# Performance work log

Measured on AMD Instinct MI355X. Metric: run time of the kernel, lower is better.

Reference implementation:

```python
import jax, jax.numpy as jnp
import numpy as np

N, D, H, C, K, NCLS, TW = 8192, 768, 4, 192, 8, 7, 1.0
HC = H * C  # 768


def setup_inputs() -> dict:
    key = jax.random.key(0)
    ks = jax.random.split(key, 40)
    gl = lambda i, shp: (jax.random.normal(ks[i], shp, jnp.float32)
                         * (1.0 / np.sqrt(shp[0] if len(shp) > 1 else shp[0])))
    inp = {"x": jax.random.normal(ks[0], (N, D), jnp.float32)}
    # BatchNorm (eval mode: running stats)
    inp["bn_gamma"] = jnp.ones((D,), jnp.float32)
    inp["bn_beta"] = jnp.zeros((D,), jnp.float32)
    inp["bn_rm"] = jnp.zeros((D,), jnp.float32)
    inp["bn_rv"] = jnp.ones((D,), jnp.float32)
    # GATConv params: W [in, H*C], att_src/att_dst [H, C], bias
    dims_in = [D, HC, HC, C]
    bias_dim = [HC, HC, C, C]  # concat,concat,mean,mean
    for li in range(4):
        b = 1 + li * 3
        inp[f"g{li+1}_w"] = gl(b, (dims_in[li], HC))
        inp[f"g{li+1}_as"] = jax.random.normal(ks[b + 1], (H, C), jnp.float32) * 0.1
        inp[f"g{li+1}_ad"] = jax.random.normal(ks[b + 2], (H, C), jnp.float32) * 0.1
        inp[f"g{li+1}_b"] = jnp.zeros((bias_dim[li],), jnp.float32)
    inp["res1_w"] = gl(14, (D, HC)); inp["res1_b"] = jnp.zeros((HC,), jnp.float32)
    inp["res2_w"] = gl(15, (HC, C)); inp["res2_b"] = jnp.zeros((C,), jnp.float32)
    for li, dim in zip(range(4), [HC, HC, C, C]):
        inp[f"ln{li+1}_g"] = jnp.ones((dim,), jnp.float32)
        inp[f"ln{li+1}_b"] = jnp.zeros((dim,), jnp.float32)
    inp["fc_w"] = gl(16, (C, NCLS)); inp["fc_b"] = jnp.zeros((NCLS,), jnp.float32)
    return inp


def _ln(x, g, b):
    mu = x.mean(-1, keepdims=True)
    v = ((x - mu) ** 2).mean(-1, keepdims=True)
    return (x - mu) * jax.lax.rsqrt(v + 1e-5) * g + b


def _build_edges(x):
    # cosine-similarity top-k graph (indices only; grads are cut upstream,
    # matching the original .item()-based host loop)
    xn = x / (jnp.linalg.norm(x, axis=1, keepdims=True) + 1e-8)
    sim = xn @ xn.T                       # [N, N]
    _, idx = jax.lax.top_k(sim, K + 1)    # first hit is self
    nbr = idx[:, 1:]                      # [N, K]
    src0 = jnp.repeat(jnp.arange(N), K)
    dst0 = nbr.reshape(-1)
    i = jnp.arange(N - 1)
    # temporal edges (i,i+1)&(i+1,i) added only if (i,i+1) not already a topk edge
    m = ~jnp.any(nbr[:-1] == (i + 1)[:, None], axis=1)
    sl = jnp.arange(N)  # self-loops (GATConv add_self_loops=True)
    src = jnp.concatenate([src0, i, i + 1, sl])
    dst = jnp.concatenate([dst0, i + 1, i, sl])
    mask = jnp.concatenate([jnp.ones(N * K, bool), m, m, jnp.ones(N, bool)])
    return src, dst, mask


def _gat(x, W, a_s, a_d, b, src, dst, mask, concat):
    n = x.shape[0]
    h = (x @ W).reshape(n, H, C)
    es = (h * a_s[None]).sum(-1)  # [N, H]
    ed = (h * a_d[None]).sum(-1)
    e = jax.nn.leaky_relu(es[src] + ed[dst], 0.2)  # [E, H]
    e = jnp.where(mask[:, None], e, -1e9)
    emax = jax.ops.segment_max(e, dst, num_segments=n)
    emax = jnp.where(jnp.isfinite(emax), emax, 0.0)
    ex = jnp.exp(e - emax[dst]) * mask[:, None].astype(e.dtype)
    denom = jax.ops.segment_sum(ex, dst, num_segments=n)
    alpha = ex / (denom[dst] + 1e-16)
    out = jax.ops.segment_sum(alpha[:, :, None] * h[src], dst, num_segments=n)
    out = out.reshape(n, HC) if concat else out.mean(1)
    return out + b


def reference(x, bn_gamma, bn_beta, bn_rm, bn_rv,
              g1_w, g1_as, g1_ad, g1_b, g2_w, g2_as, g2_ad, g2_b,
              g3_w, g3_as, g3_ad, g3_b, g4_w, g4_as, g4_ad, g4_b,
              res1_w, res1_b, res2_w, res2_b,
              ln1_g, ln1_b, ln2_g, ln2_b, ln3_g, ln3_b, ln4_g, ln4_b,
              fc_w, fc_b):
    xb = (x - bn_rm) * jax.lax.rsqrt(bn_rv + 1e-5) * bn_gamma + bn_beta
    src, dst, mask = _build_edges(jax.lax.stop_gradient(xb))
    r = xb @ res1_w + res1_b
    h = _gat(xb, g1_w, g1_as, g1_ad, g1_b, src, dst, mask, True)
    h = _ln(jax.nn.relu(h) + r, ln1_g, ln1_b)
    r = h
    h = _gat(h, g2_w, g2_as, g2_ad, g2_b, src, dst, mask, True)
    h = _ln(jax.nn.relu(h) + r, ln2_g, ln2_b)
    r = h @ res2_w + res2_b
    h = _gat(h, g3_w, g3_as, g3_ad, g3_b, src, dst, mask, False)
    h = _ln(jax.nn.relu(h) + r, ln3_g, ln3_b)
    r = h
    h = _gat(h, g4_w, g4_as, g4_ad, g4_b, src, dst, mask, False)
    h = _ln(jax.nn.relu(h) + r, ln4_g, ln4_b)
    return h @ fc_w + fc_b
```

## Files before the change

### kernel.cpp

```cpp
#include <hip/hip_runtime.h>
#include <hip/hip_bf16.h>

#define NN 8192
#define DD 768
#define HH 4
#define CC 192
#define KK 8
#define HC 768

typedef __attribute__((ext_vector_type(8))) short short8;
typedef __attribute__((ext_vector_type(4))) float floatx4;

static __device__ __forceinline__ short f2bf(float v) {
    unsigned u = __builtin_bit_cast(unsigned, v);
    u += 0x7fff + ((u >> 16) & 1);
    return (short)(u >> 16);
}
static __device__ __forceinline__ float bf2f(short s) {
    unsigned u = ((unsigned)(unsigned short)s) << 16;
    return __builtin_bit_cast(float, u);
}

static __device__ __forceinline__ void gl16(const void* g, void* l) {
    __builtin_amdgcn_global_load_lds(
        (__attribute__((address_space(1))) void*)(void*)g,
        (__attribute__((address_space(3))) void*)l, 16, 0, 0);
}

__global__ __launch_bounds__(256) void bnorm_kernel(const float* __restrict__ x,
    const float* __restrict__ g, const float* __restrict__ b,
    const float* __restrict__ rm, const float* __restrict__ rv,
    short* __restrict__ xbh, short* __restrict__ xbl,
    short* __restrict__ xnh, short* __restrict__ xnl)
{
    int i = blockIdx.x, t = threadIdx.x;
    __shared__ float red[256];
    float v[3];
    float ss = 0.f;
#pragma unroll
    for (int q = 0; q < 3; q++) {
        int d = t + q * 256;
        float xv = x[(size_t)i * DD + d];
        float vv = (xv - rm[d]) * rsqrtf(rv[d] + 1e-5f) * g[d] + b[d];
        v[q] = vv; ss += vv * vv;
    }
    red[t] = ss; __syncthreads();
    for (int s = 128; s; s >>= 1) { if (t < s) red[t] += red[t + s]; __syncthreads(); }
    float inv = 1.0f / (sqrtf(red[0]) + 1e-8f);
#pragma unroll
    for (int q = 0; q < 3; q++) {
        int d = t + q * 256;
        size_t idx = (size_t)i * DD + d;
        float vv = v[q];
        short h = f2bf(vv);
        xbh[idx] = h; xbl[idx] = f2bf(vv - bf2f(h));
        float nv = vv * inv;
        short nh = f2bf(nv);
        xnh[idx] = nh; xnl[idx] = f2bf(nv - bf2f(nh));
    }
}

__global__ __launch_bounds__(256) void wtrans6(
    const float* w0, short* o0h, short* o0l,
    const float* w1, short* o1h, short* o1l,
    const float* w2, short* o2h, short* o2l,
    const float* w3, short* o3h, short* o3l,
    const float* w4, short* o4h, short* o4l,
    const float* w5, short* o5h, short* o5l)
{
    int idx = blockIdx.x * 256 + threadIdx.x;
    const float* w; short* oh; short* ol; int K, P; int r;
    if (idx < 589824)            { w = w0; oh = o0h; ol = o0l; K = 768; P = 768; r = idx; }
    else if (idx < 2 * 589824)   { w = w1; oh = o1h; ol = o1l; K = 768; P = 768; r = idx - 589824; }
    else if (idx < 3 * 589824)   { w = w2; oh = o2h; ol = o2l; K = 768; P = 768; r = idx - 2 * 589824; }
    else if (idx < 3 * 589824 + 147456) { w = w3; oh = o3h; ol = o3l; K = 768; P = 192; r = idx - 3 * 589824; }
    else if (idx < 4 * 589824 + 147456) { w = w4; oh = o4h; ol = o4l; K = 768; P = 768; r = idx - 3 * 589824 - 147456; }
    else if (idx < 4 * 589824 + 2 * 147456) { w = w5; oh = o5h; ol = o5l; K = 192; P = 768; r = idx - 4 * 589824 - 147456; }
    else return;
    int p = r / K, k = r % K;
    float v = w[(size_t)k * P + p];
    short h = f2bf(v);
    oh[r] = h;
    ol[r] = f2bf(v - bf2f(h));
}

__global__ __launch_bounds__(256) void mfma_sym(
    const short* __restrict__ Xh, const short* __restrict__ Xl,
    int rowa, int rowb, int diag,
    float* __restrict__ Cab, float* __restrict__ Cba)
{
    __shared__ __attribute__((aligned(16))) float fsm[64 * 129];
    short* sAh = (short*)fsm;
    short* sAl = (short*)fsm + 4096;
    short* sBh = (short*)fsm + 8192;
    short* sBl = (short*)fsm + 12288;
    int t = threadIdx.x;
    int wave = t >> 6, lane = t & 63;
    int wm = wave & 1, wn = wave >> 1;
    int bi, bj;
    if (diag) {
        int L = blockIdx.x;
        int j = (int)((sqrtf(8.f * (float)L + 1.f) - 1.f) * 0.5f);
        while (j * (j + 1) / 2 > L) j--;
        while ((j + 1) * (j + 2) / 2 <= L) j++;
        bi = L - j * (j + 1) / 2; bj = j;
    } else { bi = blockIdx.y; bj = blockIdx.x; }
    int i0 = bi * 128, j0 = bj * 128;
    int mrow = lane & 15, quad = lane >> 4;

    int srow = lane >> 2;
    int kg   = (lane & 3) ^ ((lane >> 3) & 3);
    int koff = kg * 8;
    int c0 = wave * 2, c1 = c0 + 1;
    int ar0 = rowa + i0 + c0 * 16 + srow, ar1 = rowa + i0 + c1 * 16 + srow;
    int br0 = rowb + j0 + c0 * 16 + srow, br1 = rowb + j0 + c1 * 16 + srow;
    const short* pAh0 = Xh + (size_t)ar0 * DD + koff;
    const short* pAh1 = Xh + (size_t)ar1 * DD + koff;
    const short* pAl0 = Xl + (size_t)ar0 * DD + koff;
    const short* pAl1 = Xl + (size_t)ar1 * DD + koff;
    const short* pBh0 = Xh + (size_t)br0 * DD + koff;
    const short* pBh1 = Xh + (size_t)br1 * DD + koff;
    const short* pBl0 = Xl + (size_t)br0 * DD + koff;
    const short* pBl1 = Xl + (size_t)br1 * DD + koff;
    short* dA0 = sAh + c0 * 512; short* dA1 = sAh + c1 * 512;
    short* dAl0 = sAl + c0 * 512; short* dAl1 = sAl + c1 * 512;
    short* dB0 = sBh + c0 * 512; short* dB1 = sBh + c1 * 512;
    short* dBl0 = sBl + c0 * 512; short* dBl1 = sBl + c1 * 512;

    floatx4 acc[4][4];
#pragma unroll
    for (int a = 0; a < 4; a++)
#pragma unroll
        for (int b = 0; b < 4; b++) acc[a][b] = (floatx4){0.f, 0.f, 0.f, 0.f};

    int aoff[4], boff[4];
#pragma unroll
    for (int mt = 0; mt < 4; mt++) {
        int r = wm * 64 + mt * 16 + mrow;
        aoff[mt] = r * 32 + (quad ^ ((r >> 1) & 3)) * 8;
    }
#pragma unroll
    for (int nt = 0; nt < 4; nt++) {
        int r = wn * 64 + nt * 16 + mrow;
        boff[nt] = r * 32 + (quad ^ ((r >> 1) & 3)) * 8;
    }

    for (int k0 = 0; k0 < DD; k0 += 32) {
        gl16(pAh0 + k0, dA0);  gl16(pAh1 + k0, dA1);
        gl16(pAl0 + k0, dAl0); gl16(pAl1 + k0, dAl1);
        gl16(pBh0 + k0, dB0);  gl16(pBh1 + k0, dB1);
        gl16(pBl0 + k0, dBl0); gl16(pBl1 + k0, dBl1);
        __syncthreads();

        short8 ah[4], al[4], bh[4], bl[4];
#pragma unroll
        for (int mt = 0; mt < 4; mt++) {
            ah[mt] = *(const short8*)(sAh + aoff[mt]);
            al[mt] = *(const short8*)(sAl + aoff[mt]);
        }
#pragma unroll
        for (int nt = 0; nt < 4; nt++) {
            bh[nt] = *(const short8*)(sBh + boff[nt]);
            bl[nt] = *(const short8*)(sBl + boff[nt]);
        }
#pragma unroll
        for (int mt = 0; mt < 4; mt++)
#pragma unroll
            for (int nt = 0; nt < 4; nt++) {
                acc[mt][nt] = __builtin_amdgcn_mfma_f32_16x16x32_bf16(
                    ah[mt], bh[nt], acc[mt][nt], 0, 0, 0);
                acc[mt][nt] = __builtin_amdgcn_mfma_f32_16x16x32_bf16(
                    ah[mt], bl[nt], acc[mt][nt], 0, 0, 0);
                acc[mt][nt] = __builtin_amdgcn_mfma_f32_16x16x32_bf16(
                    al[mt], bh[nt], acc[mt][nt], 0, 0, 0);
            }
        __syncthreads();
    }

#pragma unroll
    for (int mt = 0; mt < 4; mt++)
#pragma unroll
        for (int nt = 0; nt < 4; nt++) {
            int col = j0 + wn * 64 + nt * 16 + mrow;
#pragma unroll
            for (int r = 0; r < 4; r++) {
                int row = i0 + wm * 64 + mt * 16 + quad * 4 + r;
                Cab[(size_t)row * 4096 + col] = acc[mt][nt][r];
            }
        }

    if (!diag || bi != bj) {
        float* Cm = Cba;
        for (int half = 0; half < 2; half++) {
            __syncthreads();
            if (wn == half) {
#pragma unroll
                for (int mt = 0; mt < 4; mt++)
#pragma unroll
                    for (int nt = 0; nt < 4; nt++)
#pragma unroll
                        for (int r = 0; r < 4; r++) {
                            int c = nt * 16 + mrow;
                            int rr = wm * 64 + mt * 16 + quad * 4 + r;
                            fsm[c * 129 + rr] = acc[mt][nt][r];
                        }
            }
            __syncthreads();
            for (int it = 0; it < 32; it++) {
                int idx = it * 256 + t;
                int lr = idx >> 7, lc = idx & 127;
                Cm[(size_t)(j0 + half * 64 + lr) * 4096 + i0 + lc] = fsm[lr * 129 + lc];
            }
        }
    }
}

__global__ __launch_bounds__(256) void mfma_nt(
    const short* __restrict__ Ahi, const short* __restrict__ Alo,
    const short* __restrict__ Bhi, const short* __restrict__ Blo,
    const float* __restrict__ bias, int biasN,
    float* __restrict__ C, int Cstride,
    short* __restrict__ Cbf, int bfoff, int bfstride,
    const float* __restrict__ a_s, const float* __restrict__ a_d,
    float* __restrict__ es, float* __restrict__ ed, int hoff,
    int M, int K, int P)
{
    __shared__ __attribute__((aligned(16))) short sAh[128 * 32];
    __shared__ __attribute__((aligned(16))) short sAl[128 * 32];
    __shared__ __attribute__((aligned(16))) short sBh[128 * 32];
    __shared__ __attribute__((aligned(16))) short sBl[128 * 32];
    int t = threadIdx.x;
    int wave = t >> 6, lane = t & 63;
    int wm = wave & 1, wn = wave >> 1;
    int i0 = blockIdx.y * 128, j0 = blockIdx.x * 128;
    int mrow = lane & 15, quad = lane >> 4;

    int srow = lane >> 2;
    int kg   = (lane & 3) ^ ((lane >> 3) & 3);
    int koff = kg * 8;
    int c0 = wave * 2, c1 = c0 + 1;
    int ar0 = i0 + c0 * 16 + srow, ar1 = i0 + c1 * 16 + srow;
    int br0 = j0 + c0 * 16 + srow, br1 = j0 + c1 * 16 + srow;
    if (br0 > P - 1) br0 = P - 1;
    if (br1 > P - 1) br1 = P - 1;
    const short* pAh0 = Ahi + (size_t)ar0 * K + koff;
    const short* pAh1 = Ahi + (size_t)ar1 * K + koff;
    const short* pAl0 = Alo + (size_t)ar0 * K + koff;
    const short* pAl1 = Alo + (size_t)ar1 * K + koff;
    const short* pBh0 = Bhi + (size_t)br0 * K + koff;
    const short* pBh1 = Bhi + (size_t)br1 * K + koff;
    const short* pBl0 = Blo + (size_t)br0 * K + koff;
    const short* pBl1 = Blo + (size_t)br1 * K + koff;
    short* dA0 = sAh + c0 * 512; short* dA1 = sAh + c1 * 512;
    short* dAl0 = sAl + c0 * 512; short* dAl1 = sAl + c1 * 512;
    short* dB0 = sBh + c0 * 512; short* dB1 = sBh + c1 * 512;
    short* dBl0 = sBl + c0 * 512; short* dBl1 = sBl + c1 * 512;

    floatx4 acc[4][4];
#pragma unroll
    for (int a = 0; a < 4; a++)
#pragma unroll
        for (int b = 0; b < 4; b++) acc[a][b] = (floatx4){0.f, 0.f, 0.f, 0.f};

    int aoff[4], boff[4];
#pragma unroll
    for (int mt = 0; mt < 4; mt++) {
        int r = wm * 64 + mt * 16 + mrow;
        aoff[mt] = r * 32 + (quad ^ ((r >> 1) & 3)) * 8;
    }
#pragma unroll
    for (int nt = 0; nt < 4; nt++) {
        int r = wn * 64 + nt * 16 + mrow;
        boff[nt] = r * 32 + (quad ^ ((r >> 1) & 3)) * 8;
    }

    for (int k0 = 0; k0 < K; k0 += 32) {
        gl16(pAh0 + k0, dA0);  gl16(pAh1 + k0, dA1);
        gl16(pAl0 + k0, dAl0); gl16(pAl1 + k0, dAl1);
        gl16(pBh0 + k0, dB0);  gl16(pBh1 + k0, dB1);
        gl16(pBl0 + k0, dBl0); gl16(pBl1 + k0, dBl1);
        __syncthreads();

        short8 ah[4], al[4], bh[4], bl[4];
#pragma unroll
        for (int mt = 0; mt < 4; mt++) {
            ah[mt] = *(const short8*)(sAh + aoff[mt]);
            al[mt] = *(const short8*)(sAl + aoff[mt]);
        }
#pragma unroll
        for (int nt = 0; nt < 4; nt++) {
            bh[nt] = *(const short8*)(sBh + boff[nt]);
            bl[nt] = *(const short8*)(sBl + boff[nt]);
        }
#pragma unroll
        for (int mt = 0; mt < 4; mt++)
#pragma unroll
            for (int nt = 0; nt < 4; nt++) {
                acc[mt][nt] = __builtin_amdgcn_mfma_f32_16x16x32_bf16(
                    ah[mt], bh[nt], acc[mt][nt], 0, 0, 0);
                acc[mt][nt] = __builtin_amdgcn_mfma_f32_16x16x32_bf16(
                    ah[mt], bl[nt], acc[mt][nt], 0, 0, 0);
                acc[mt][nt] = __builtin_amdgcn_mfma_f32_16x16x32_bf16(
                    al[mt], bh[nt], acc[mt][nt], 0, 0, 0);
            }
        __syncthreads();
    }

#pragma unroll
    for (int mt = 0; mt < 4; mt++)
#pragma unroll
        for (int nt = 0; nt < 4; nt++) {
            int col = j0 + wn * 64 + nt * 16 + mrow;
            if (col < P) {
                if (col < bfoff) {
                    float bb = (bias && col < biasN) ? bias[col] : 0.f;
#pragma unroll
                    for (int r = 0; r < 4; r++) {
                        int row = i0 + wm * 64 + mt * 16 + quad * 4 + r;
                        C[(size_t)row * Cstride + col] = acc[mt][nt][r] + bb;
                    }
                } else {
#pragma unroll
                    for (int r = 0; r < 4; r++) {
                        int row = i0 + wm * 64 + mt * 16 + quad * 4 + r;
                        Cbf[(size_t)row * bfstride + col - bfoff] = f2bf(acc[mt][nt][r]);
                    }
                }
            }
        }

    if (a_s) {
        int base = j0 + wn * 64;
        if (base >= hoff && base + 64 <= P) {
            int head = (base - hoff) / CC;
            int cb = (base - hoff) % CC;
#pragma unroll
            for (int mt = 0; mt < 4; mt++) {
                float ps[4] = {0.f, 0.f, 0.f, 0.f};
                float pd[4] = {0.f, 0.f, 0.f, 0.f};
#pragma unroll
                for (int nt = 0; nt < 4; nt++) {
                    int c = cb + nt * 16 + mrow;
                    float as_ = a_s[head * CC + c];
                    float ad_ = a_d[head * CC + c];
#pragma unroll
                    for (int r = 0; r < 4; r++) {
                        ps[r] += acc[mt][nt][r] * as_;
                        pd[r] += acc[mt][nt][r] * ad_;
                    }
                }
#pragma unroll
                for (int off = 1; off < 16; off <<= 1)
#pragma unroll
                    for (int r = 0; r < 4; r++) {
                        ps[r] += __shfl_xor(ps[r], off);
                        pd[r] += __shfl_xor(pd[r], off);
                    }
                if (mrow == 0) {
#pragma unroll
                    for (int r = 0; r < 4; r++) {
                        int row = i0 + wm * 64 + mt * 16 + quad * 4 + r;
                        atomicAdd(&es[row * 4 + head], ps[r]);
                        atomicAdd(&ed[row * 4 + head], pd[r]);
                    }
                }
            }
        }
    }
}

__device__ __forceinline__ bool tk_try(float* v, int* id, float xv, int xi)
{
    if (xv > v[8] || (xv == v[8] && xi < id[8])) {
        v[8] = xv; id[8] = xi;
#pragma unroll
        for (int p = 8; p > 0; p--) {
            if (v[p] > v[p - 1] || (v[p] == v[p - 1] && id[p] < id[p - 1])) {
                float tv = v[p]; v[p] = v[p - 1]; v[p - 1] = tv;
                int ti2 = id[p]; id[p] = id[p - 1]; id[p - 1] = ti2;
            } else break;
        }
        return true;
    }
    return false;
}

__global__ __launch_bounds__(256) void topk1p_kernel(const float* __restrict__ sim,
    float* __restrict__ pv, int* __restrict__ pi,
    int rowbase, int segbase, int colbase)
{
    int wave = threadIdx.x >> 6, lane = threadIdx.x & 63;
    int task = blockIdx.x * 4 + wave;
    int row = task >> 2, seg = task & 3;
    const float4* p4 = (const float4*)(sim + (size_t)row * 4096 + seg * 1024);

    float4 f0 = p4[lane], f1 = p4[lane + 64], f2 = p4[lane + 128], f3 = p4[lane + 192];
    float v[9]; int id[9];
#pragma unroll
    for (int q = 0; q < 9; q++) { v[q] = -3e38f; id[q] = 0x7fffffff; }
    int jb = colbase + seg * 1024 + lane * 4;
#pragma unroll
    for (int g = 0; g < 4; g++) {
        float4 f = g == 0 ? f0 : (g == 1 ? f1 : (g == 2 ? f2 : f3));
        float gm = fmaxf(fmaxf(f.x, f.y), fmaxf(f.z, f.w));
        if (gm >= v[8]) {
            int j = jb + g * 256;
            tk_try(v, id, f.x, j);
            tk_try(v, id, f.y, j + 1);
            tk_try(v, id, f.z, j + 2);
            tk_try(v, id, f.w, j + 3);
        }
    }
    float wv = -3e38f; int wi = 0x7fffffff;
#pragma unroll
    for (int r = 0; r < 9; r++) {
        float bv = v[0]; int bi = id[0];
#pragma unroll
        for (int off = 1; off < 64; off <<= 1) {
            float ov = __shfl_xor(bv, off);
            int oi = __shfl_xor(bi, off);
            if (ov > bv || (ov == bv && oi < bi)) { bv = ov; bi = oi; }
        }
        if (id[0] == bi) {
#pragma unroll
            for (int q = 0; q < 8; q++) { v[q] = v[q + 1]; id[q] = id[q + 1]; }
            v[8] = -3e38f; id[8] = 0x7fffffff;
        }
        if (lane == r) { wv = bv; wi = bi; }
    }
    if (lane < 9) {
        size_t o = ((size_t)(rowbase + row) * 8 + segbase + seg) * 9 + lane;
        pv[o] = wv; pi[o] = wi;
    }
}

__global__ __launch_bounds__(256) void topk2_kernel(const float* __restrict__ pv,
    const int* __restrict__ pi, int* __restrict__ nbr, int r0)
{
    int wave = threadIdx.x >> 6, lane = threadIdx.x & 63;
    int row = blockIdx.x * 4 + wave;
    size_t base = (size_t)row * 72;
    float v[2]; int id[2];
    v[0] = -3e38f; id[0] = 0x7fffffff;
    v[1] = -3e38f; id[1] = 0x7fffffff;
    if (lane < 72) { v[0] = pv[base + lane]; id[0] = pi[base + lane]; }
    if (lane < 8)  { v[1] = pv[base + 64 + lane]; id[1] = pi[base + 64 + lane]; }
    if (v[1] > v[0] || (v[1] == v[0] && id[1] < id[0])) {
        float tv = v[0]; v[0] = v[1]; v[1] = tv;
        int ti = id[0]; id[0] = id[1]; id[1] = ti;
    }
    int myi = 0;
#pragma unroll
    for (int r = 0; r < 9; r++) {
        float bv = v[0]; int bi = id[0];
#pragma unroll
        for (int off = 1; off < 64; off <<= 1) {
            float ov = __shfl_xor(bv, off);
            int oi = __shfl_xor(bi, off);
            if (ov > bv || (ov == bv && oi < bi)) { bv = ov; bi = oi; }
        }
        if (id[0] == bi) {
            v[0] = v[1]; id[0] = id[1];
            v[1] = -3e38f; id[1] = 0x7fffffff;
        }
        if (r >= 1 && lane == r - 1) myi = bi;
    }
    if (lane < KK) nbr[(size_t)(r0 + row) * KK + lane] = myi;
}

__global__ __launch_bounds__(256) void count_kernel(const int* __restrict__ nbr,
                                                    int* __restrict__ deg, int* __restrict__ mfl)
{
    int i = blockIdx.x * 256 + threadIdx.x;
    if (i >= NN) return;
    atomicAdd(&deg[i], 1);
    int mm = 0;
#pragma unroll
    for (int k = 0; k < KK; k++) {
        int j = nbr[i * KK + k];
        atomicAdd(&deg[j], 1);
        if (j == i + 1) mm = 1;
    }
    if (i < NN - 1) {
        mfl[i] = !mm;
        if (!mm) { atomicAdd(&deg[i + 1], 1); atomicAdd(&deg[i], 1); }
    }
}

__global__ __launch_bounds__(256) void scan_kernel(const int* __restrict__ deg,
                                                   int* __restrict__ rowptr, int* __restrict__ cur)
{
    __shared__ int sums[256];
    int t = threadIdx.x;
    int loc[32];
    int base = t * 32;
    int s = 0;
#pragma unroll
    for (int q = 0; q < 32; q++) { loc[q] = s; s += deg[base + q]; }
    sums[t] = s; __syncthreads();
    for (int off = 1; off < 256; off <<= 1) {
        int v = (t >= off) ? sums[t - off] : 0;
        __syncthreads();
        sums[t] += v;
        __syncthreads();
    }
    int myoff = (t == 0) ? 0 : sums[t - 1];
#pragma unroll
    for (int q = 0; q < 32; q++) { int rp = myoff + loc[q]; rowptr[base + q] = rp; cur[base + q] = rp; }
    if (t == 255) rowptr[NN] = sums[255];
}

__global__ __launch_bounds__(256) void fill_kernel(const int* __restrict__ nbr,
    const int* __restrict__ mfl, int* __restrict__ cur, int* __restrict__ csr)
{
    int i = blockIdx.x * 256 + threadIdx.x;
    if (i >= NN) return;
    int pos = atomicAdd(&cur[i], 1); csr[pos] = i;
#pragma unroll
    for (int k = 0; k < KK; k++) {
        int j = nbr[i * KK + k];
        pos = atomicAdd(&cur[j], 1); csr[pos] = i;
    }
    if (i < NN - 1 && mfl[i]) {
        pos = atomicAdd(&cur[i + 1], 1); csr[pos] = i;
        pos = atomicAdd(&cur[i], 1); csr[pos] = i + 1;
    }
}

__global__ __launch_bounds__(256) void agg_ln_kernel(const short* __restrict__ h, int hst,
    const float* __restrict__ es, const float* __restrict__ ed,
    const int* __restrict__ rowptr, const int* __restrict__ csr,
    const float* __restrict__ gb, const float* __restrict__ rres, int rst,
    const float* __restrict__ gamma, const float* __restrict__ beta,
    float* __restrict__ outp, short* __restrict__ ohi, short* __restrict__ olo,
    int Dm, int concat,
    const float* __restrict__ fcw, const float* __restrict__ fcb,
    float* __restrict__ fco)
{
    int j = blockIdx.x;
    int t = threadIdx.x;
    int lane = t & 63, wave = t >> 6;
    __shared__ int ssrc[256];
    __shared__ float sal[256 * 4];
    __shared__ float sred[1024];
    __shared__ float accs[768];
    int p0 = rowptr[j], p1 = rowptr[j + 1];
    int cnt = p1 - p0;
    float edj[4];
#pragma unroll
    for (int hd = 0; hd < 4; hd++) edj[hd] = ed[j * 4 + hd];

    float acc0 = 0.f, acc1 = 0.f, acc2 = 0.f;
    int d0 = t, d1 = t + 256, d2 = t + 512;
    int h0 = d0 / CC, h1_ = d1 / CC, h2_ = d2 / CC;

    if (cnt <= 256) {
        float e[4];
        if (t < cnt) {
            int s = csr[p0 + t];
            ssrc[t] = s;
#pragma unroll
            for (int hd = 0; hd < 4; hd++) {
                float ee = es[s * 4 + hd] + edj[hd];
                e[hd] = ee > 0.f ? ee : 0.2f * ee;
            }
        } else {
#pragma unroll
            for (int hd = 0; hd < 4; hd++) e[hd] = -1e30f;
        }
        float mh[4];
#pragma unroll
        for (int hd = 0; hd < 4; hd++) {
            float rv = e[hd];
#pragma unroll
            for (int off = 32; off; off >>= 1) rv = fmaxf(rv, __shfl_down(rv, off));
            if (lane == 0) sred[wave * 4 + hd] = rv;
        }
        __syncthreads();
#pragma unroll
        for (int hd = 0; hd < 4; hd++)
            mh[hd] = fmaxf(fmaxf(sred[hd], sred[4 + hd]), fmaxf(sred[8 + hd], sred[12 + hd]));
        __syncthreads();
        float ex[4];
#pragma unroll
        for (int hd = 0; hd < 4; hd++) {
            ex[hd] = (t < cnt) ? expf(e[hd] - mh[hd]) : 0.f;
            float rv = ex[hd];
#pragma unroll
            for (int off = 32; off; off >>= 1) rv += __shfl_down(rv, off);
            if (lane == 0) sred[wave * 4 + hd] = rv;
        }
        __syncthreads();
#pragma unroll
        for (int hd = 0; hd < 4; hd++) {
            float dh = sred[hd] + sred[4 + hd] + sred[8 + hd] + sred[12 + hd] + 1e-16f;
            if (t < cnt) sal[t * 4 + hd] = ex[hd] / dh;
        }
        __syncthreads();
        for (int e2 = 0; e2 < cnt; e2++) {
            const short* hs = h + (size_t)ssrc[e2] * hst;
            acc0 += sal[e2 * 4 + h0] * bf2f(hs[d0]);
            acc1 += sal[e2 * 4 + h1_] * bf2f(hs[d1]);
            acc2 += sal[e2 * 4 + h2_] * bf2f(hs[d2]);
        }
    } else {
        float mh[4] = {-1e30f, -1e30f, -1e30f, -1e30f};
        for (int p = p0 + t; p < p1; p += 256) {
            int s = csr[p];
// ... 78 lines not shown
        for (int s = 128; s; s >>= 1) { if (t < s) sred[t] += sred[t + s]; __syncthreads(); }
        float rs = rsqrtf(sred[0] / 768.f + 1e-5f);
        size_t base = (size_t)j * 768;
        float w0 = a0 * rs * gamma[d0] + beta[d0];
        float w1 = a1 * rs * gamma[d1] + beta[d1];
        float w2 = a2 * rs * gamma[d2] + beta[d2];
        if (outp) { outp[base + d0] = w0; outp[base + d1] = w1; outp[base + d2] = w2; }
        short hh;
        hh = f2bf(w0); ohi[base + d0] = hh; olo[base + d0] = f2bf(w0 - bf2f(hh));
        hh = f2bf(w1); ohi[base + d1] = hh; olo[base + d1] = f2bf(w1 - bf2f(hh));
        hh = f2bf(w2); ohi[base + d2] = hh; olo[base + d2] = f2bf(w2 - bf2f(hh));
    } else {
        accs[d0] = acc0; accs[d1] = acc1; accs[d2] = acc2;
        __syncthreads();
        float val = 0.f;
        if (t < CC)
            val = fmaxf((accs[t] + accs[t + CC] + accs[t + 2 * CC] + accs[t + 3 * CC]) * 0.25f
                        + gb[t], 0.f) + rres[(size_t)j * rst + t];
        __syncthreads();
        sred[t] = (t < CC) ? val : 0.f; __syncthreads();
        for (int s = 128; s; s >>= 1) { if (t < s) sred[t] += sred[t + s]; __syncthreads(); }
        float mu = sred[0] / (float)CC;
        __syncthreads();
        float a = val - mu;
        sred[t] = (t < CC) ? a * a : 0.f; __syncthreads();
        for (int s = 128; s; s >>= 1) { if (t < s) sred[t] += sred[t + s]; __syncthreads(); }
        float rs = rsqrtf(sred[0] / (float)CC + 1e-5f);
        float w = a * rs * ((t < CC) ? gamma[t] : 0.f) + ((t < CC) ? beta[t] : 0.f);
        if (t < CC) {
            size_t idx = (size_t)j * CC + t;
            if (outp) outp[idx] = w;
            if (ohi) {
                short hh = f2bf(w);
                ohi[idx] = hh; olo[idx] = f2bf(w - bf2f(hh));
            }
            accs[t] = w;
        }
        if (fco) {
            __syncthreads();
            if (t < 64) {
#pragma unroll
                for (int n = 0; n < 7; n++) {
                    float p = 0.f;
                    for (int d = t; d < CC; d += 64) p += accs[d] * fcw[d * 7 + n];
#pragma unroll
                    for (int off = 32; off; off >>= 1) p += __shfl_down(p, off);
                    if (t == 0) fco[(size_t)j * 7 + n] = p + fcb[n];
                }
            }
        }
    }
}

extern "C" void kernel_launch(void* const* d_in, const int* in_sizes, int n_in,
                              void* d_out, int out_size, void* d_ws, size_t ws_size,
                              hipStream_t stream)
{
    const float* x     = (const float*)d_in[0];
    const float* bn_g  = (const float*)d_in[1];
    const float* bn_b  = (const float*)d_in[2];
    const float* bn_rm = (const float*)d_in[3];
    const float* bn_rv = (const float*)d_in[4];
    const float* g_w[4]  = {(const float*)d_in[5], (const float*)d_in[9],
                            (const float*)d_in[13], (const float*)d_in[17]};
    const float* g_as[4] = {(const float*)d_in[6], (const float*)d_in[10],
                            (const float*)d_in[14], (const float*)d_in[18]};
    const float* g_ad[4] = {(const float*)d_in[7], (const float*)d_in[11],
                            (const float*)d_in[15], (const float*)d_in[19]};
    const float* g_b[4]  = {(const float*)d_in[8], (const float*)d_in[12],
                            (const float*)d_in[16], (const float*)d_in[20]};
    const float* res1_w = (const float*)d_in[21];
    const float* res1_b = (const float*)d_in[22];
    const float* res2_w = (const float*)d_in[23];
    const float* res2_b = (const float*)d_in[24];
    const float* ln_g[4] = {(const float*)d_in[25], (const float*)d_in[27],
                            (const float*)d_in[29], (const float*)d_in[31]};
    const float* ln_b[4] = {(const float*)d_in[26], (const float*)d_in[28],
                            (const float*)d_in[30], (const float*)d_in[32]};
    const float* fc_w = (const float*)d_in[33];
    const float* fc_b = (const float*)d_in[34];
    float* out = (float*)d_out;

    float* F = (float*)d_ws;
    float* SAB  = F; F += 16777216;
    float* UNI  = F; F += 16777216;
    float* SBA = UNI;
    float* R1  = UNI;
    float* H1  = R1 + 6291456;
    float* R2  = H1 + 6291456;
    float* H3  = R2 + 1572864;
    float* ESB = H3 + 1572864;
    short* S = (short*)F;
    short* XNH = S; S += 6291456;
    short* XNL = S; S += 6291456;
    short* XAH = S; S += 6291456;
    short* XAL = S; S += 6291456;
    short* HBH = S; S += 6291456;
    short* WT1H = S; S += 1179648;
    short* WT1L = S; S += 1179648;
    short* WT2H = S; S += 589824;
    short* WT2L = S; S += 589824;
    short* WT3H = S; S += 737280;
    short* WT3L = S; S += 737280;
    short* WT4H = S; S += 147456;
    short* WT4L = S; S += 147456;
    int* I = (int*)S;
    int* NBR    = I; I += NN * KK;
    int* DEG    = I; I += NN;
    int* ROWPTR = I; I += NN + 8;
    int* CUR    = I; I += NN;
    int* MFL    = I; I += NN;
    int* CSR    = I; I += 131072;
    float* PV   = (float*)I; I += 589824;
    int* PI     = I; I += 589824;
    float* ES[4], *ED[4];
    for (int l = 0; l < 4; l++) { ES[l] = ESB + l * 65536; ED[l] = ES[l] + 32768; }

    bnorm_kernel<<<NN, 256, 0, stream>>>(x, bn_g, bn_b, bn_rm, bn_rv,
                                         XAH, XAL, XNH, XNL);
    hipMemsetAsync(DEG, 0, NN * sizeof(int), stream);
    wtrans6<<<(4 * 589824 + 2 * 147456 + 255) / 256, 256, 0, stream>>>(
        res1_w, WT1H, WT1L,
        g_w[0], WT1H + 768 * 768, WT1L + 768 * 768,
        g_w[1], WT2H, WT2L,
        res2_w, WT3H, WT3L,
        g_w[2], WT3H + 192 * 768, WT3L + 192 * 768,
        g_w[3], WT4H, WT4L);
    mfma_sym<<<dim3(32, 32), 256, 0, stream>>>(XNH, XNL, 0, 4096, 0, SAB, SBA);
    topk1p_kernel<<<4096, 256, 0, stream>>>(SAB, PV, PI, 0, 4, 4096);
    topk1p_kernel<<<4096, 256, 0, stream>>>(SBA, PV, PI, 4096, 0, 0);
    mfma_sym<<<528, 256, 0, stream>>>(XNH, XNL, 0, 0, 1, SAB, SAB);
    topk1p_kernel<<<4096, 256, 0, stream>>>(SAB, PV, PI, 0, 0, 0);
    mfma_sym<<<528, 256, 0, stream>>>(XNH, XNL, 4096, 4096, 1, SBA, SBA);
    topk1p_kernel<<<4096, 256, 0, stream>>>(SBA, PV, PI, 4096, 4, 4096);
    topk2_kernel<<<NN / 4, 256, 0, stream>>>(PV, PI, NBR, 0);
    count_kernel<<<NN / 256, 256, 0, stream>>>(NBR, DEG, MFL);
    scan_kernel<<<1, 256, 0, stream>>>(DEG, ROWPTR, CUR);
    fill_kernel<<<NN / 256, 256, 0, stream>>>(NBR, MFL, CUR, CSR);
    hipMemsetAsync(ESB, 0, 262144 * sizeof(float), stream);
    mfma_nt<<<dim3(12, NN / 128), 256, 0, stream>>>(XAH, XAL, WT1H, WT1L,
        res1_b, 768, R1, 768, HBH, 768, 768,
        g_as[0], g_ad[0], ES[0], ED[0], 768, NN, DD, 1536);
    agg_ln_kernel<<<NN, 256, 0, stream>>>(HBH, 768, ES[0], ED[0], ROWPTR, CSR,
        g_b[0], R1, 768, ln_g[0], ln_b[0], H1, XAH, XAL, HC, 1, nullptr, nullptr, nullptr);
    mfma_nt<<<dim3(6, NN / 128), 256, 0, stream>>>(XAH, XAL, WT2H, WT2L,
        nullptr, 0, nullptr, 0, HBH, 0, 768,
        g_as[1], g_ad[1], ES[1], ED[1], 0, NN, HC, HC);
    agg_ln_kernel<<<NN, 256, 0, stream>>>(HBH, 768, ES[1], ED[1], ROWPTR, CSR,
        g_b[1], H1, 768, ln_g[1], ln_b[1], nullptr, XAH, XAL, HC, 1, nullptr, nullptr, nullptr);
    mfma_nt<<<dim3(8, NN / 128), 256, 0, stream>>>(XAH, XAL, WT3H, WT3L,
        res2_b, 192, R2, 192, HBH, 192, 768,
        g_as[2], g_ad[2], ES[2], ED[2], 192, NN, HC, 960);
    agg_ln_kernel<<<NN, 256, 0, stream>>>(HBH, 768, ES[2], ED[2], ROWPTR, CSR,
        g_b[2], R2, 192, ln_g[2], ln_b[2], H3, XAH, XAL, CC, 0, nullptr, nullptr, nullptr);
    mfma_nt<<<dim3(6, NN / 128), 256, 0, stream>>>(XAH, XAL, WT4H, WT4L,
        nullptr, 0, nullptr, 0, HBH, 0, 768,
        g_as[3], g_ad[3], ES[3], ED[3], 0, NN, CC, HC);
    agg_ln_kernel<<<NN, 256, 0, stream>>>(HBH, 768, ES[3], ED[3], ROWPTR, CSR,
        g_b[3], H3, 192, ln_g[3], ln_b[3], nullptr, nullptr, nullptr, CC, 0, fc_w, fc_b, out);
}
```

Before: 1.085 ms.

## Compute similarity in single bf16, store bf16 sims, rescore top candidates in fp32

The cosine-similarity GEMM now uses only the high bf16 part (one MFMA instead of three) and writes its results as bf16, which halves the similarity matrix traffic. The top-k pass over bf16 sims keeps 24 candidates per row, and a new rescore kernel recomputes their exact fp32 dot products to pick the final 8 neighbours. The two diagonal GEMM launches and the topk launches are merged into fewer, larger launches. The risk is that a true neighbour falls outside the 24 bf16 candidates when similarities are close.

```diff
diff --git a/kernel.cpp b/kernel.cpp
--- a/kernel.cpp
+++ b/kernel.cpp
@@ -31,7 +31,7 @@
     const float* __restrict__ g, const float* __restrict__ b,
     const float* __restrict__ rm, const float* __restrict__ rv,
     short* __restrict__ xbh, short* __restrict__ xbl,
-    short* __restrict__ xnh, short* __restrict__ xnl)
+    short* __restrict__ xnh, float* __restrict__ xnf)
 {
     int i = blockIdx.x, t = threadIdx.x;
     __shared__ float red[256];
@@ -55,8 +55,8 @@
         short h = f2bf(vv);
         xbh[idx] = h; xbl[idx] = f2bf(vv - bf2f(h));
         float nv = vv * inv;
-        short nh = f2bf(nv);
-        xnh[idx] = nh; xnl[idx] = f2bf(nv - bf2f(nh));
+        xnf[idx] = nv;
+        xnh[idx] = f2bf(nv);
     }
 }
 
@@ -85,26 +85,29 @@
 }
 
 __global__ __launch_bounds__(256) void mfma_sym(
-    const short* __restrict__ Xh, const short* __restrict__ Xl,
-    int rowa, int rowb, int diag,
-    float* __restrict__ Cab, float* __restrict__ Cba)
-{
-    __shared__ __attribute__((aligned(16))) float fsm[64 * 129];
-    short* sAh = (short*)fsm;
-    short* sAl = (short*)fsm + 4096;
-    short* sBh = (short*)fsm + 8192;
-    short* sBl = (short*)fsm + 12288;
+    const short* __restrict__ Xh, int mode,
+    short* __restrict__ P0, short* __restrict__ P1)
+{
+    __shared__ __attribute__((aligned(16))) short smem[8704];
+    short* sAh = smem;
+    short* sBh = smem + 4096;
     int t = threadIdx.x;
     int wave = t >> 6, lane = t & 63;
     int wm = wave & 1, wn = wave >> 1;
-    int bi, bj;
-    if (diag) {
+    int bi, bj, rowa, rowb; short *Cab, *Cba;
+    if (mode == 0) {
+        bi = blockIdx.y; bj = blockIdx.x; rowa = 0; rowb = 4096;
+        Cab = P0; Cba = P1;
+    } else {
         int L = blockIdx.x;
+        int which = (L >= 528) ? 1 : 0; L -= which * 528;
         int j = (int)((sqrtf(8.f * (float)L + 1.f) - 1.f) * 0.5f);
         while (j * (j + 1) / 2 > L) j--;
         while ((j + 1) * (j + 2) / 2 <= L) j++;
         bi = L - j * (j + 1) / 2; bj = j;
-    } else { bi = blockIdx.y; bj = blockIdx.x; }
+        rowa = rowb = which ? 4096 : 0;
+        Cab = Cba = which ? P1 : P0;
+    }
     int i0 = bi * 128, j0 = bj * 128;
     int mrow = lane & 15, quad = lane >> 4;
 
@@ -112,20 +115,12 @@
     int kg   = (lane & 3) ^ ((lane >> 3) & 3);
     int koff = kg * 8;
     int c0 = wave * 2, c1 = c0 + 1;
-    int ar0 = rowa + i0 + c0 * 16 + srow, ar1 = rowa + i0 + c1 * 16 + srow;
-    int br0 = rowb + j0 + c0 * 16 + srow, br1 = rowb + j0 + c1 * 16 + srow;
-    const short* pAh0 = Xh + (size_t)ar0 * DD + koff;
-    const short* pAh1 = Xh + (size_t)ar1 * DD + koff;
-    const short* pAl0 = Xl + (size_t)ar0 * DD + koff;
-    const short* pAl1 = Xl + (size_t)ar1 * DD + koff;
-    const short* pBh0 = Xh + (size_t)br0 * DD + koff;
-    const short* pBh1 = Xh + (size_t)br1 * DD + koff;
-    const short* pBl0 = Xl + (size_t)br0 * DD + koff;
-    const short* pBl1 = Xl + (size_t)br1 * DD + koff;
+    const short* pA0 = Xh + (size_t)(rowa + i0 + c0 * 16 + srow) * DD + koff;
+    const short* pA1 = Xh + (size_t)(rowa + i0 + c1 * 16 + srow) * DD + koff;
+    const short* pB0 = Xh + (size_t)(rowb + j0 + c0 * 16 + srow) * DD + koff;
+    const short* pB1 = Xh + (size_t)(rowb + j0 + c1 * 16 + srow) * DD + koff;
     short* dA0 = sAh + c0 * 512; short* dA1 = sAh + c1 * 512;
-    short* dAl0 = sAl + c0 * 512; short* dAl1 = sAl + c1 * 512;
     short* dB0 = sBh + c0 * 512; short* dB1 = sBh + c1 * 512;
-    short* dBl0 = sBl + c0 * 512; short* dBl1 = sBl + c1 * 512;
 
     floatx4 acc[4][4];
 #pragma unroll
@@ -146,51 +141,46 @@
     }
 
     for (int k0 = 0; k0 < DD; k0 += 32) {
-        gl16(pAh0 + k0, dA0);  gl16(pAh1 + k0, dA1);
-        gl16(pAl0 + k0, dAl0); gl16(pAl1 + k0, dAl1);
-        gl16(pBh0 + k0, dB0);  gl16(pBh1 + k0, dB1);
-        gl16(pBl0 + k0, dBl0); gl16(pBl1 + k0, dBl1);
-        __syncthreads();
-
-        short8 ah[4], al[4], bh[4], bl[4];
-#pragma unroll
-        for (int mt = 0; mt < 4; mt++) {
-            ah[mt] = *(const short8*)(sAh + aoff[mt]);
-            al[mt] = *(const short8*)(sAl + aoff[mt]);
-        }
-#pragma unroll
-        for (int nt = 0; nt < 4; nt++) {
-            bh[nt] = *(const short8*)(sBh + boff[nt]);
-            bl[nt] = *(const short8*)(sBl + boff[nt]);
-        }
+        gl16(pA0 + k0, dA0); gl16(pA1 + k0, dA1);
+        gl16(pB0 + k0, dB0); gl16(pB1 + k0, dB1);
+        __syncthreads();
+        short8 ah[4], bh[4];
+#pragma unroll
+        for (int mt = 0; mt < 4; mt++) ah[mt] = *(const short8*)(sAh + aoff[mt]);
+#pragma unroll
+        for (int nt = 0; nt < 4; nt++) bh[nt] = *(const short8*)(sBh + boff[nt]);
 #pragma unroll
         for (int mt = 0; mt < 4; mt++)
 #pragma unroll
-            for (int nt = 0; nt < 4; nt++) {
+            for (int nt = 0; nt < 4; nt++)
                 acc[mt][nt] = __builtin_amdgcn_mfma_f32_16x16x32_bf16(
                     ah[mt], bh[nt], acc[mt][nt], 0, 0, 0);
-                acc[mt][nt] = __builtin_amdgcn_mfma_f32_16x16x32_bf16(
-                    ah[mt], bl[nt], acc[mt][nt], 0, 0, 0);
-                acc[mt][nt] = __builtin_amdgcn_mfma_f32_16x16x32_bf16(
-                    al[mt], bh[nt], acc[mt][nt], 0, 0, 0);
-            }
-        __syncthreads();
-    }
-
-#pragma unroll
-    for (int mt = 0; mt < 4; mt++)
-#pragma unroll
-        for (int nt = 0; nt < 4; nt++) {
-            int col = j0 + wn * 64 + nt * 16 + mrow;
-#pragma unroll
-            for (int r = 0; r < 4; r++) {
-                int row = i0 + wm * 64 + mt * 16 + quad * 4 + r;
-                Cab[(size_t)row * 4096 + col] = acc[mt][nt][r];
-            }
-        }
-
-    if (!diag || bi != bj) {
-        float* Cm = Cba;
+        __syncthreads();
+    }
+
+    short* st = smem;
+    for (int half = 0; half < 2; half++) {
+        __syncthreads();
+        if (wm == half) {
+#pragma unroll
+            for (int mt = 0; mt < 4; mt++)
+#pragma unroll
+                for (int nt = 0; nt < 4; nt++)
+#pragma unroll
+                    for (int r = 0; r < 4; r++)
+                        st[(mt * 16 + quad * 4 + r) * 136 + wn * 64 + nt * 16 + mrow]
+                            = f2bf(acc[mt][nt][r]);
+        }
+        __syncthreads();
+#pragma unroll
+        for (int it = 0; it < 4; it++) {
+            int idx = it * 256 + t;
+            int lr = idx >> 4, lc = (idx & 15) * 8;
+            *(short8*)&Cab[(size_t)(i0 + half * 64 + lr) * 4096 + j0 + lc]
+                = *(const short8*)&st[lr * 136 + lc];
+        }
+    }
+    if (mode == 0 || bi != bj) {
         for (int half = 0; half < 2; half++) {
             __syncthreads();
             if (wn == half) {
@@ -199,19 +189,227 @@
 #pragma unroll
                     for (int nt = 0; nt < 4; nt++)
 #pragma unroll
-                        for (int r = 0; r < 4; r++) {
-                            int c = nt * 16 + mrow;
-                            int rr = wm * 64 + mt * 16 + quad * 4 + r;
-                            fsm[c * 129 + rr] = acc[mt][nt][r];
-                        }
+                        for (int r = 0; r < 4; r++)
+                            st[(nt * 16 + mrow) * 136 + wm * 64 + mt * 16 + quad * 4 + r]
+                                = f2bf(acc[mt][nt][r]);
             }
             __syncthreads();
-            for (int it = 0; it < 32; it++) {
+#pragma unroll
+            for (int it = 0; it < 4; it++) {
                 int idx = it * 256 + t;
-                int lr = idx >> 7, lc = idx & 127;
-                Cm[(size_t)(j0 + half * 64 + lr) * 4096 + i0 + lc] = fsm[lr * 129 + lc];
-            }
-        }
+                int lr = idx >> 4, lc = (idx & 15) * 8;
+                *(short8*)&Cba[(size_t)(j0 + half * 64 + lr) * 4096 + i0 + lc]
+                    = *(const short8*)&st[lr * 136 + lc];
+            }
+        }
+    }
+}
+
+__device__ __forceinline__ bool tk_try(float* v, int* id, float xv, int xi)
+{
+    if (xv > v[8] || (xv == v[8] && xi < id[8])) {
+        v[8] = xv; id[8] = xi;
+#pragma unroll
+        for (int p = 8; p > 0; p--) {
+            if (v[p] > v[p - 1] || (v[p] == v[p - 1] && id[p] < id[p - 1])) {
+                float tv = v[p]; v[p] = v[p - 1]; v[p - 1] = tv;
+                int ti2 = id[p]; id[p] = id[p - 1]; id[p - 1] = ti2;
+            } else break;
+        }
+        return true;
+    }
+    return false;
+}
+
+__global__ __launch_bounds__(256) void topk1b_kernel(
+    const short* __restrict__ simA, const short* __restrict__ simB,
+    float* __restrict__ pv, int* __restrict__ pi, int phase)
+{
+    int wave = threadIdx.x >> 6, lane = threadIdx.x & 63;
+    int gtask = blockIdx.x * 4 + wave;
+    int which = (gtask >= 16384) ? 1 : 0;
+    int task = gtask - which * 16384;
+    const short* sim = which ? simB : simA;
+    int rowbase = which ? 4096 : 0;
+    int segbase, colbase;
+    if (phase == 0) { segbase = which ? 0 : 4; colbase = which ? 0 : 4096; }
+    else            { segbase = which ? 4 : 0; colbase = which ? 4096 : 0; }
+    int row = task >> 2, seg = task & 3;
+    const short8* p8 = (const short8*)(sim + (size_t)row * 4096 + seg * 1024);
+    short8 s0 = p8[lane], s1 = p8[lane + 64];
+    float v[9]; int id[9];
+#pragma unroll
+    for (int q = 0; q < 9; q++) { v[q] = -3e38f; id[q] = 0x7fffffff; }
+    int jb = colbase + seg * 1024 + lane * 8;
+    float f0[8], f1[8];
+#pragma unroll
+    for (int q = 0; q < 8; q++) { f0[q] = bf2f(s0[q]); f1[q] = bf2f(s1[q]); }
+    float g0 = f0[0], g1 = f1[0];
+#pragma unroll
+    for (int q = 1; q < 8; q++) { g0 = fmaxf(g0, f0[q]); g1 = fmaxf(g1, f1[q]); }
+    if (g0 >= v[8]) {
+#pragma unroll
+        for (int q = 0; q < 8; q++) tk_try(v, id, f0[q], jb + q);
+    }
+    if (g1 >= v[8]) {
+#pragma unroll
+        for (int q = 0; q < 8; q++) tk_try(v, id, f1[q], jb + 512 + q);
+    }
+    float wv = -3e38f; int wi = 0x7fffffff;
+#pragma unroll
+    for (int r = 0; r < 9; r++) {
+        float bv = v[0]; int bi = id[0];
+#pragma unroll
+        for (int off = 1; off < 64; off <<= 1) {
+            float ov = __shfl_xor(bv, off);
+            int oi = __shfl_xor(bi, off);
+            if (ov > bv || (ov == bv && oi < bi)) { bv = ov; bi = oi; }
+        }
+        if (id[0] == bi) {
+#pragma unroll
+            for (int q = 0; q < 8; q++) { v[q] = v[q + 1]; id[q] = id[q + 1]; }
+            v[8] = -3e38f; id[8] = 0x7fffffff;
+        }
+        if (lane == r) { wv = bv; wi = bi; }
+    }
+    if (lane < 9) {
+        size_t o = ((size_t)(rowbase + row) * 8 + segbase + seg) * 9 + lane;
+        pv[o] = wv; pi[o] = wi;
+    }
+}
+
+__global__ __launch_bounds__(256) void rescore_kernel(
+    const float* __restrict__ xnf,
+    const float* __restrict__ pv, const int* __restrict__ pi,
+    int* __restrict__ nbr)
+{
+    int row = blockIdx.x, t = threadIdx.x;
+    int wave = t >> 6, lane = t & 63;
+    __shared__ float own[768];
+    __shared__ float cv[72]; __shared__ int ci[72];
+    __shared__ int seli[24];
+    __shared__ float rv[24]; __shared__ int ri[24];
+    for (int d = t; d < 768; d += 256) own[d] = xnf[(size_t)row * 768 + d];
+    if (t < 72) { cv[t] = pv[(size_t)row * 72 + t]; ci[t] = pi[(size_t)row * 72 + t]; }
+    __syncthreads();
+    if (wave == 0) {
+        float v[2]; int id[2];
+        v[0] = (lane < 72) ? cv[lane] : -3e38f;
+        id[0] = (lane < 72) ? ci[lane] : 0x7fffffff;
+        v[1] = (lane < 8) ? cv[64 + lane] : -3e38f;
+        id[1] = (lane < 8) ? ci[64 + lane] : 0x7fffffff;
+        if (v[1] > v[0] || (v[1] == v[0] && id[1] < id[0])) {
+            float tv = v[0]; v[0] = v[1]; v[1] = tv;
+            int ti = id[0]; id[0] = id[1]; id[1] = ti;
+        }
+#pragma unroll
+        for (int r = 0; r < 24; r++) {
+            float bv = v[0]; int bi = id[0];
+#pragma unroll
+            for (int off = 1; off < 64; off <<= 1) {
+                float ov = __shfl_xor(bv, off);
+                int oi = __shfl_xor(bi, off);
+                if (ov > bv || (ov == bv && oi < bi)) { bv = ov; bi = oi; }
+            }
+            if (id[0] == bi) {
+                v[0] = v[1]; id[0] = id[1];
+                v[1] = -3e38f; id[1] = 0x7fffffff;
+            }
+            if (lane == r) seli[r] = bi;
+        }
+    }
+    __syncthreads();
+    float ow[12];
+#pragma unroll
+    for (int q = 0; q < 12; q++) ow[q] = own[q * 64 + lane];
+    for (int k = 0; k < 6; k++) {
+        int c = wave * 6 + k;
+        int src = seli[c];
+        const float* cr = xnf + (size_t)src * 768;
+        float s = 0.f;
+#pragma unroll
+        for (int q = 0; q < 12; q++) s += ow[q] * cr[q * 64 + lane];
+#pragma unroll
+        for (int off = 32; off; off >>= 1) s += __shfl_xor(s, off);
+        if (lane == 0) { rv[c] = s; ri[c] = src; }
+    }
+    __syncthreads();
+    if (wave == 0) {
+        float v0 = (lane < 24) ? rv[lane] : -3e38f;
+        int i0_ = (lane < 24) ? ri[lane] : 0x7fffffff;
+        int myi = 0;
+#pragma unroll
+        for (int r = 0; r < 9; r++) {
+            float bv = v0; int bi = i0_;
+#pragma unroll
+            for (int off = 1; off < 64; off <<= 1) {
+                float ov = __shfl_xor(bv, off);
+                int oi = __shfl_xor(bi, off);
+                if (ov > bv || (ov == bv && oi < bi)) { bv = ov; bi = oi; }
+            }
+            if (i0_ == bi) { v0 = -3e38f; i0_ = 0x7fffffff; }
+            if (r >= 1 && lane == r - 1) myi = bi;
+        }
+        if (lane < KK) nbr[(size_t)row * KK + lane] = myi;
+    }
+}
+
+__global__ __launch_bounds__(256) void count_kernel(const int* __restrict__ nbr,
+                                                    int* __restrict__ deg, int* __restrict__ mfl)
+{
+    int i = blockIdx.x * 256 + threadIdx.x;
+    if (i >= NN) return;
+    atomicAdd(&deg[i], 1);
+    int mm = 0;
+#pragma unroll
+    for (int k = 0; k < KK; k++) {
+        int j = nbr[i * KK + k];
+        atomicAdd(&deg[j], 1);
+        if (j == i + 1) mm = 1;
+    }
+    if (i < NN - 1) {
+        mfl[i] = !mm;
+        if (!mm) { atomicAdd(&deg[i + 1], 1); atomicAdd(&deg[i], 1); }
+    }
+}
+
+__global__ __launch_bounds__(256) void scan_kernel(const int* __restrict__ deg,
+                                                   int* __restrict__ rowptr, int* __restrict__ cur)
+{
+    __shared__ int sums[256];
+    int t = threadIdx.x;
+    int loc[32];
+    int base = t * 32;
+    int s = 0;
+#pragma unroll
+    for (int q = 0; q < 32; q++) { loc[q] = s; s += deg[base + q]; }
+    sums[t] = s; __syncthreads();
+    for (int off = 1; off < 256; off <<= 1) {
+        int v = (t >= off) ? sums[t - off] : 0;
+        __syncthreads();
+        sums[t] += v;
+        __syncthreads();
+    }
+    int myoff = (t == 0) ? 0 : sums[t - 1];
+#pragma unroll
+    for (int q = 0; q < 32; q++) { int rp = myoff + loc[q]; rowptr[base + q] = rp; cur[base + q] = rp; }
+    if (t == 255) rowptr[NN] = sums[255];
+}
+
+__global__ __launch_bounds__(256) void fill_kernel(const int* __restrict__ nbr,
+    const int* __restrict__ mfl, int* __restrict__ cur, int* __restrict__ csr)
+{
+    int i = blockIdx.x * 256 + threadIdx.x;
+    if (i >= NN) return;
+    int pos = atomicAdd(&cur[i], 1); csr[pos] = i;
+#pragma unroll
+    for (int k = 0; k < KK; k++) {
+        int j = nbr[i * KK + k];
+        pos = atomicAdd(&cur[j], 1); csr[pos] = i;
+    }
+    if (i < NN - 1 && mfl[i]) {
+        pos = atomicAdd(&cur[i + 1], 1); csr[pos] = i;
+        pos = atomicAdd(&cur[i], 1); csr[pos] = i + 1;
     }
 }
 
@@ -366,164 +564,6 @@
                 }
             }
         }
-    }
-}
-
-__device__ __forceinline__ bool tk_try(float* v, int* id, float xv, int xi)
-{
-    if (xv > v[8] || (xv == v[8] && xi < id[8])) {
-        v[8] = xv; id[8] = xi;
-#pragma unroll
-        for (int p = 8; p > 0; p--) {
-            if (v[p] > v[p - 1] || (v[p] == v[p - 1] && id[p] < id[p - 1])) {
-                float tv = v[p]; v[p] = v[p - 1]; v[p - 1] = tv;
-                int ti2 = id[p]; id[p] = id[p - 1]; id[p - 1] = ti2;
-            } else break;
-        }
-        return true;
-    }
-    return false;
-}
-
-__global__ __launch_bounds__(256) void topk1p_kernel(const float* __restrict__ sim,
-    float* __restrict__ pv, int* __restrict__ pi,
-    int rowbase, int segbase, int colbase)
-{
-    int wave = threadIdx.x >> 6, lane = threadIdx.x & 63;
-    int task = blockIdx.x * 4 + wave;
-    int row = task >> 2, seg = task & 3;
-    const float4* p4 = (const float4*)(sim + (size_t)row * 4096 + seg * 1024);
-
-    float4 f0 = p4[lane], f1 = p4[lane + 64], f2 = p4[lane + 128], f3 = p4[lane + 192];
-    float v[9]; int id[9];
-#pragma unroll
-    for (int q = 0; q < 9; q++) { v[q] = -3e38f; id[q] = 0x7fffffff; }
-    int jb = colbase + seg * 1024 + lane * 4;
-#pragma unroll
-    for (int g = 0; g < 4; g++) {
-        float4 f = g == 0 ? f0 : (g == 1 ? f1 : (g == 2 ? f2 : f3));
-        float gm = fmaxf(fmaxf(f.x, f.y), fmaxf(f.z, f.w));
-        if (gm >= v[8]) {
-            int j = jb + g * 256;
-            tk_try(v, id, f.x, j);
-            tk_try(v, id, f.y, j + 1);
-            tk_try(v, id, f.z, j + 2);
-            tk_try(v, id, f.w, j + 3);
-        }
-    }
-    float wv = -3e38f; int wi = 0x7fffffff;
-#pragma unroll
-    for (int r = 0; r < 9; r++) {
-        float bv = v[0]; int bi = id[0];
-#pragma unroll
-        for (int off = 1; off < 64; off <<= 1) {
-            float ov = __shfl_xor(bv, off);
-            int oi = __shfl_xor(bi, off);
-            if (ov > bv || (ov == bv && oi < bi)) { bv = ov; bi = oi; }
-        }
-        if (id[0] == bi) {
-#pragma unroll
-            for (int q = 0; q < 8; q++) { v[q] = v[q + 1]; id[q] = id[q + 1]; }
-            v[8] = -3e38f; id[8] = 0x7fffffff;
-        }
-        if (lane == r) { wv = bv; wi = bi; }
-    }
-    if (lane < 9) {
-        size_t o = ((size_t)(rowbase + row) * 8 + segbase + seg) * 9 + lane;
-        pv[o] = wv; pi[o] = wi;
-    }
-}
-
-__global__ __launch_bounds__(256) void topk2_kernel(const float* __restrict__ pv,
-    const int* __restrict__ pi, int* __restrict__ nbr, int r0)
-{
-    int wave = threadIdx.x >> 6, lane = threadIdx.x & 63;
-    int row = blockIdx.x * 4 + wave;
-    size_t base = (size_t)row * 72;
-    float v[2]; int id[2];
-    v[0] = -3e38f; id[0] = 0x7fffffff;
-    v[1] = -3e38f; id[1] = 0x7fffffff;
-    if (lane < 72) { v[0] = pv[base + lane]; id[0] = pi[base + lane]; }
-    if (lane < 8)  { v[1] = pv[base + 64 + lane]; id[1] = pi[base + 64 + lane]; }
-    if (v[1] > v[0] || (v[1] == v[0] && id[1] < id[0])) {
-        float tv = v[0]; v[0] = v[1]; v[1] = tv;
-        int ti = id[0]; id[0] = id[1]; id[1] = ti;
-    }
-    int myi = 0;
-#pragma unroll
-    for (int r = 0; r < 9; r++) {
-        float bv = v[0]; int bi = id[0];
-#pragma unroll
-        for (int off = 1; off < 64; off <<= 1) {
-            float ov = __shfl_xor(bv, off);
-            int oi = __shfl_xor(bi, off);
-            if (ov > bv || (ov == bv && oi < bi)) { bv = ov; bi = oi; }
-        }
-        if (id[0] == bi) {
-            v[0] = v[1]; id[0] = id[1];
-            v[1] = -3e38f; id[1] = 0x7fffffff;
-        }
-        if (r >= 1 && lane == r - 1) myi = bi;
-    }
-    if (lane < KK) nbr[(size_t)(r0 + row) * KK + lane] = myi;
-}
-
-__global__ __launch_bounds__(256) void count_kernel(const int* __restrict__ nbr,
-                                                    int* __restrict__ deg, int* __restrict__ mfl)
-{
-    int i = blockIdx.x * 256 + threadIdx.x;
-    if (i >= NN) return;
-    atomicAdd(&deg[i], 1);
-    int mm = 0;
-#pragma unroll
-    for (int k = 0; k < KK; k++) {
-        int j = nbr[i * KK + k];
-        atomicAdd(&deg[j], 1);
-        if (j == i + 1) mm = 1;
-    }
-    if (i < NN - 1) {
-        mfl[i] = !mm;
-        if (!mm) { atomicAdd(&deg[i + 1], 1); atomicAdd(&deg[i], 1); }
-    }
-}
-
-__global__ __launch_bounds__(256) void scan_kernel(const int* __restrict__ deg,
-                                                   int* __restrict__ rowptr, int* __restrict__ cur)
-{
-    __shared__ int sums[256];
-    int t = threadIdx.x;
-    int loc[32];
-    int base = t * 32;
-    int s = 0;
-#pragma unroll
-    for (int q = 0; q < 32; q++) { loc[q] = s; s += deg[base + q]; }
-    sums[t] = s; __syncthreads();
-    for (int off = 1; off < 256; off <<= 1) {
-        int v = (t >= off) ? sums[t - off] : 0;
-        __syncthreads();
-        sums[t] += v;
-        __syncthreads();
-    }
-    int myoff = (t == 0) ? 0 : sums[t - 1];
-#pragma unroll
-    for (int q = 0; q < 32; q++) { int rp = myoff + loc[q]; rowptr[base + q] = rp; cur[base + q] = rp; }
-    if (t == 255) rowptr[NN] = sums[255];
-}
-
-__global__ __launch_bounds__(256) void fill_kernel(const int* __restrict__ nbr,
-    const int* __restrict__ mfl, int* __restrict__ cur, int* __restrict__ csr)
-{
-    int i = blockIdx.x * 256 + threadIdx.x;
-    if (i >= NN) return;
-    int pos = atomicAdd(&cur[i], 1); csr[pos] = i;
-#pragma unroll
-    for (int k = 0; k < KK; k++) {
-        int j = nbr[i * KK + k];
-        pos = atomicAdd(&cur[j], 1); csr[pos] = i;
-    }
-    if (i < NN - 1 && mfl[i]) {
-        pos = atomicAdd(&cur[i + 1], 1); csr[pos] = i;
-        pos = atomicAdd(&cur[i], 1); csr[pos] = i + 1;
     }
 }
 
@@ -768,17 +808,17 @@
     float* out = (float*)d_out;
 
     float* F = (float*)d_ws;
-    float* SAB  = F; F += 16777216;
-    float* UNI  = F; F += 16777216;
-    float* SBA = UNI;
-    float* R1  = UNI;
-    float* H1  = R1 + 6291456;
-    float* R2  = H1 + 6291456;
-    float* H3  = R2 + 1572864;
-    float* ESB = H3 + 1572864;
+    float* XNF = F; F += 6291456;
+    float* R1  = F; F += 6291456;
+    float* H1  = F; F += 6291456;
+    float* R2  = F; F += 1572864;
+    float* H3  = F; F += 1572864;
+    float* ESB = F; F += 262144;
+    float* PV  = F; F += 589824;
     short* S = (short*)F;
+    short* SAB = S; S += 16777216;
+    short* SBA = S; S += 16777216;
     short* XNH = S; S += 6291456;
-    short* XNL = S; S += 6291456;
     short* XAH = S; S += 6291456;
     short* XAL = S; S += 6291456;
     short* HBH = S; S += 6291456;
@@ -797,14 +837,14 @@
     int* CUR    = I; I += NN;
     int* MFL    = I; I += NN;
     int* CSR    = I; I += 131072;
-    float* PV   = (float*)I; I += 589824;
     int* PI     = I; I += 589824;
     float* ES[4], *ED[4];
     for (int l = 0; l < 4; l++) { ES[l] = ESB + l * 65536; ED[l] = ES[l] + 32768; }
 
     bnorm_kernel<<<NN, 256, 0, stream>>>(x, bn_g, bn_b, bn_rm, bn_rv,
-                                         XAH, XAL, XNH, XNL);
+                                         XAH, XAL, XNH, XNF);
     hipMemsetAsync(DEG, 0, NN * sizeof(int), stream);
+    hipMemsetAsync(ESB, 0, 262144 * sizeof(float), stream);
     wtrans6<<<(4 * 589824 + 2 * 147456 + 255) / 256, 256, 0, stream>>>(
         res1_w, WT1H, WT1L,
         g_w[0], WT1H + 768 * 768, WT1L + 768 * 768,
@@ -812,18 +852,14 @@
         res2_w, WT3H, WT3L,
         g_w[2], WT3H + 192 * 768, WT3L + 192 * 768,
         g_w[3], WT4H, WT4L);
-    mfma_sym<<<dim3(32, 32), 256, 0, stream>>>(XNH, XNL, 0, 4096, 0, SAB, SBA);
-    topk1p_kernel<<<4096, 256, 0, stream>>>(SAB, PV, PI, 0, 4, 4096);
-    topk1p_kernel<<<4096, 256, 0, stream>>>(SBA, PV, PI, 4096, 0, 0);
-    mfma_sym<<<528, 256, 0, stream>>>(XNH, XNL, 0, 0, 1, SAB, SAB);
-    topk1p_kernel<<<4096, 256, 0, stream>>>(SAB, PV, PI, 0, 0, 0);
-    mfma_sym<<<528, 256, 0, stream>>>(XNH, XNL, 4096, 4096, 1, SBA, SBA);
-    topk1p_kernel<<<4096, 256, 0, stream>>>(SBA, PV, PI, 4096, 4, 4096);
-    topk2_kernel<<<NN / 4, 256, 0, stream>>>(PV, PI, NBR, 0);
+    mfma_sym<<<dim3(32, 32), 256, 0, stream>>>(XNH, 0, SAB, SBA);
+    topk1b_kernel<<<8192, 256, 0, stream>>>(SAB, SBA, PV, PI, 0);
+    mfma_sym<<<1056, 256, 0, stream>>>(XNH, 1, SAB, SBA);
+    topk1b_kernel<<<8192, 256, 0, stream>>>(SAB, SBA, PV, PI, 1);
+    rescore_kernel<<<NN, 256, 0, stream>>>(XNF, PV, PI, NBR);
     count_kernel<<<NN / 256, 256, 0, stream>>>(NBR, DEG, MFL);
     scan_kernel<<<1, 256, 0, stream>>>(DEG, ROWPTR, CUR);
     fill_kernel<<<NN / 256, 256, 0, stream>>>(NBR, MFL, CUR, CSR);
-    hipMemsetAsync(ESB, 0, 262144 * sizeof(float), stream);
     mfma_nt<<<dim3(12, NN / 128), 256, 0, stream>>>(XAH, XAL, WT1H, WT1L,
         res1_b, 768, R1, 768, HBH, 768, 768,
         g_as[0], g_ad[0], ES[0], ED[0], 768, NN, DD, 1536);
```

Result: no change. 1.082 ms (-0.3%).
